# Kernel optimization log

Measured on AMD Instinct MI355X. Metric: run time of the kernel, lower is better.

## Reference

```python
import jax, jax.numpy as jnp
import numpy as np

B, T, D, H, C = 64, 256, 512, 1024, 1000

def setup_inputs() -> dict:
    key = jax.random.key(0)
    ks = jax.random.split(key, 6)
    s = 1.0 / np.sqrt(H)  # torch nn.RNN init scale
    return {
        "x": jax.random.normal(ks[0], (B, T, D), dtype=jnp.float32),
        "w_ih0": jax.random.normal(ks[1], (H, D), dtype=jnp.float32) * s,
        "w_hh0": jax.random.normal(ks[2], (H, H), dtype=jnp.float32) * s,
        "w_ih1": jax.random.normal(ks[3], (H, H), dtype=jnp.float32) * s,
        "w_hh1": jax.random.normal(ks[4], (H, H), dtype=jnp.float32) * s,
        "w_fc": jax.random.normal(ks[5], (C, H), dtype=jnp.float32) * s,
    }

def _rnn_layer(inp, w_ih, w_hh):
    # inp: [B, T, Din]; ReLU RNN, no bias (matches nn.RNN(nonlinearity='relu', bias=False))
    xs = jnp.einsum('btd,hd->tbh', inp, w_ih)  # precompute input projections for all steps
    h0 = jnp.zeros((inp.shape[0], w_hh.shape[0]), dtype=inp.dtype)
    def step(h, x_t):
        h = jax.nn.relu(x_t + h @ w_hh.T)
        return h, h
    _, ys = jax.lax.scan(step, h0, xs)  # ys: [T, B, H]
    return jnp.swapaxes(ys, 0, 1)  # [B, T, H]

def reference(x, w_ih0, w_hh0, w_ih1, w_hh1, w_fc):
    h1 = _rnn_layer(x, w_ih0, w_hh0)
    h2 = _rnn_layer(h1, w_ih1, w_hh1)
    # fc on last timestep, no bias
    return h2[:, -1, :] @ w_fc.T  # [B, C]
```

## Files before the change

### kernel.cpp

```cpp
#include <hip/hip_runtime.h>

#define T_STEPS 256
#define BATCH   64
#define HID     1024
#define DIN     512
#define NCLS    1000
#define NBLK    128
#define HSZ     (BATCH * HID)

typedef __attribute__((ext_vector_type(8))) short  short8;
typedef __attribute__((ext_vector_type(4))) float  f32x4;

__device__ __forceinline__ unsigned short rne_bf16(float f) {
    unsigned int u = __builtin_bit_cast(unsigned int, f);
    u += 0x7FFFu + ((u >> 16) & 1u);
    return (unsigned short)(u >> 16);
}
__device__ __forceinline__ float bf16_to_f(unsigned short h) {
    unsigned int u = ((unsigned int)h) << 16;
    return __builtin_bit_cast(float, u);
}

#define MFMA(a, b, c) __builtin_amdgcn_mfma_f32_16x16x32_bf16((a), (b), (c), 0, 0, 0)

__device__ __forceinline__ void grid_bar(int* cnt, int* gen, int bid, int tid, int p) {
    __syncthreads();
    if (tid == 0) {
        __threadfence();
        __hip_atomic_fetch_add(&cnt[(bid & 7) * 32], 1,
                               __ATOMIC_RELAXED, __HIP_MEMORY_SCOPE_AGENT);
        if (bid == 0) {
            const int target = NBLK * (p + 1);
            for (long it = 0; it < 1000000L; ++it) {
                int s = 0;
#pragma unroll
                for (int i = 0; i < 8; ++i)
                    s += __hip_atomic_load(&cnt[i * 32], __ATOMIC_RELAXED,
                                           __HIP_MEMORY_SCOPE_AGENT);
                if (s >= target) break;
                __builtin_amdgcn_s_sleep(1);
            }
            __threadfence();
            __hip_atomic_store(gen, p + 1, __ATOMIC_RELAXED, __HIP_MEMORY_SCOPE_AGENT);
        } else {
            for (long it = 0; it < 1000000L; ++it) {
                if (__hip_atomic_load(gen, __ATOMIC_RELAXED,
                                      __HIP_MEMORY_SCOPE_AGENT) >= p + 1)
                    break;
                __builtin_amdgcn_s_sleep(1);
            }
            __threadfence();
        }
    }
    __syncthreads();
}

__device__ __forceinline__ void reduce_store(const float* red, int tid,
                                             int mbase, int nbase,
                                             unsigned short* ohi, unsigned short* olo,
                                             float* of, const float* xp) {
    const int m = tid >> 4;
    const int n = (tid * 2) & 31;
    float s0, s1;
    if (xp) {
        float2 xi = *(const float2*)(xp + (size_t)(mbase + m) * HID + nbase + n);
        s0 = xi.x; s1 = xi.y;
    } else { s0 = 0.f; s1 = 0.f; }
#pragma unroll
    for (int ww = 0; ww < 8; ++ww) {
        const float* rp = red + ww * 1088 + m * 34 + n;
        s0 += rp[0];
        s1 += rp[1];
    }
    const float v0 = fmaxf(s0, 0.f), v1 = fmaxf(s1, 0.f);
    const unsigned short h0 = rne_bf16(v0), h1 = rne_bf16(v1);
    const unsigned int hp = (unsigned int)h0 | ((unsigned int)h1 << 16);
    const unsigned int lp = (unsigned int)rne_bf16(v0 - bf16_to_f(h0)) |
                            ((unsigned int)rne_bf16(v1 - bf16_to_f(h1)) << 16);
    const size_t o = (size_t)(mbase + m) * HID + nbase + n;
    *(unsigned int*)(ohi + o) = hp;
    *(unsigned int*)(olo + o) = lp;
    if (of) { float2 f2; f2.x = v0; f2.y = v1; *(float2*)(of + o) = f2; }
}

__global__ __launch_bounds__(512, 2)
void rnn_mfma(const float* __restrict__ xproj,
              const unsigned short* __restrict__ whh0h, const unsigned short* __restrict__ whh0l,
              const unsigned short* __restrict__ wih1h, const unsigned short* __restrict__ wih1l,
              const unsigned short* __restrict__ whh1h, const unsigned short* __restrict__ whh1l,
              unsigned short* h1hi, unsigned short* h1lo,
              unsigned short* h2hi, unsigned short* h2lo,
              float* h2f, int* bar) {
    __shared__ float red[8 * 1088];

    const int bid   = blockIdx.x;
    const int z     = bid >> 6;
    const int r     = bid & 63;
    const int nbase = (r >> 1) * 32;
    const int mbase = (r & 1) * 32;
    const int tid   = threadIdx.x;
    const int w     = tid >> 6;
    const int lane  = tid & 63;
    const int l15   = lane & 15;
    const int kq    = (lane >> 4) * 8;

    int* cnt = bar;
    int* gen = bar + 256;

    if (z == 0) {
        short8 WH[2][4], WL[2][4];
        const int kb = w * 128;
#pragma unroll
        for (int c = 0; c < 4; ++c)
#pragma unroll
            for (int nt = 0; nt < 2; ++nt) {
                const size_t o = (size_t)(nbase + nt * 16 + l15) * HID + kb + c * 32 + kq;
                WH[nt][c] = *(const short8*)(whh0h + o);
                WL[nt][c] = *(const short8*)(whh0l + o);
            }
        for (int p = 0; p <= T_STEPS; ++p) {
            if (p < T_STEPS) {
                f32x4 acc[2][2] = {};
                const unsigned short* hch = h1hi + (size_t)(p & 1) * HSZ;
                const unsigned short* hcl = h1lo + (size_t)(p & 1) * HSZ;
#pragma unroll
                for (int c = 0; c < 4; ++c) {
                    short8 ah[2], al[2];
#pragma unroll
                    for (int mt = 0; mt < 2; ++mt) {
                        const size_t o = (size_t)(mbase + mt * 16 + l15) * HID + kb + c * 32 + kq;
                        ah[mt] = *(const short8*)(hch + o);
                        al[mt] = *(const short8*)(hcl + o);
                    }
#pragma unroll
                    for (int mt = 0; mt < 2; ++mt)
#pragma unroll
                        for (int nt = 0; nt < 2; ++nt) {
                            acc[mt][nt] = MFMA(ah[mt], WH[nt][c], acc[mt][nt]);
                            acc[mt][nt] = MFMA(al[mt], WH[nt][c], acc[mt][nt]);
                            acc[mt][nt] = MFMA(ah[mt], WL[nt][c], acc[mt][nt]);
                        }
                }
#pragma unroll
                for (int mt = 0; mt < 2; ++mt)
#pragma unroll
                    for (int nt = 0; nt < 2; ++nt)
#pragma unroll
                        for (int i = 0; i < 4; ++i)
                            red[w * 1088 + (mt * 16 + (lane >> 4) * 4 + i) * 34 +
                                nt * 16 + l15] = acc[mt][nt][i];
                __syncthreads();
                const size_t ob = (size_t)((p + 1) & 1) * HSZ;
                reduce_store(red, tid, mbase, nbase, h1hi + ob, h1lo + ob, nullptr,
                             xproj + (size_t)p * BATCH * HID);
            }
            grid_bar(cnt, gen, bid, tid, p);
        }
    } else {
        short8 WH[2][8], WL[2][8];
        const unsigned short* ph = (w < 4) ? wih1h : whh1h;
        const unsigned short* pl = (w < 4) ? wih1l : whh1l;
        const int kb = (w & 3) * 256;
#pragma unroll
        for (int c = 0; c < 8; ++c)
#pragma unroll
            for (int nt = 0; nt < 2; ++nt) {
                const size_t o = (size_t)(nbase + nt * 16 + l15) * HID + kb + c * 32 + kq;
                WH[nt][c] = *(const short8*)(ph + o);
                WL[nt][c] = *(const short8*)(pl + o);
            }
        for (int p = 0; p <= T_STEPS; ++p) {
            if (p >= 1) {
                f32x4 acc[2][2] = {};
                const unsigned short* ash = (w < 4) ? h1hi + (size_t)(p & 1) * HSZ
                                                    : h2hi + (size_t)((p - 1) & 1) * HSZ;
                const unsigned short* asl = (w < 4) ? h1lo + (size_t)(p & 1) * HSZ
                                                    : h2lo + (size_t)((p - 1) & 1) * HSZ;
#pragma unroll
                for (int c = 0; c < 8; ++c) {
                    short8 ah[2], al[2];
#pragma unroll
                    for (int mt = 0; mt < 2; ++mt) {
                        const size_t o = (size_t)(mbase + mt * 16 + l15) * HID + kb + c * 32 + kq;
                        ah[mt] = *(const short8*)(ash + o);
                        al[mt] = *(const short8*)(asl + o);
                    }
#pragma unroll
                    for (int mt = 0; mt < 2; ++mt)
#pragma unroll
                        for (int nt = 0; nt < 2; ++nt) {
                            acc[mt][nt] = MFMA(ah[mt], WH[nt][c], acc[mt][nt]);
                            acc[mt][nt] = MFMA(al[mt], WH[nt][c], acc[mt][nt]);
                            acc[mt][nt] = MFMA(ah[mt], WL[nt][c], acc[mt][nt]);
                        }
                }
#pragma unroll
                for (int mt = 0; mt < 2; ++mt)
#pragma unroll
                    for (int nt = 0; nt < 2; ++nt)
#pragma unroll
                        for (int i = 0; i < 4; ++i)
                            red[w * 1088 + (mt * 16 + (lane >> 4) * 4 + i) * 34 +
                                nt * 16 + l15] = acc[mt][nt][i];
                __syncthreads();
                const size_t ob = (size_t)(p & 1) * HSZ;
                reduce_store(red, tid, mbase, nbase, h2hi + ob, h2lo + ob,
                             (p == T_STEPS) ? h2f : nullptr, nullptr);
            }
            grid_bar(cnt, gen, bid, tid, p);
        }
    }
}

__global__ __launch_bounds__(512)
void xproj_gemm(const float* __restrict__ x,
                const unsigned short* __restrict__ wh,
                const unsigned short* __restrict__ wl,
                float* __restrict__ xproj) {
    const int t    = blockIdx.x;
    const int nq   = blockIdx.y;
    const int w    = threadIdx.x >> 6;
    const int lane = threadIdx.x & 63;
    const int l15  = lane & 15;
    const int kq   = (lane >> 4) * 8;
    const int n0   = nq * 256 + w * 32;

    f32x4 acc[4][2] = {};
    for (int c = 0; c < 16; ++c) {
        const int k = c * 32 + kq;
        short8 wfh[2], wfl[2];
#pragma unroll
        for (int nt = 0; nt < 2; ++nt) {
            const size_t o = (size_t)(n0 + nt * 16 + l15) * DIN + k;
            wfh[nt] = *(const short8*)(wh + o);
            wfl[nt] = *(const short8*)(wl + o);
        }
#pragma unroll
        for (int mt = 0; mt < 4; ++mt) {
            const float* xr = x + ((size_t)(mt * 16 + l15) * T_STEPS + t) * DIN + k;
            float4 a0 = *(const float4*)xr;
            float4 a1 = *(const float4*)(xr + 4);
            float f[8] = {a0.x, a0.y, a0.z, a0.w, a1.x, a1.y, a1.z, a1.w};
            short8 ah, al;
#pragma unroll
            for (int i = 0; i < 8; ++i) {
                unsigned short h = rne_bf16(f[i]);
                ah[i] = (short)h;
                al[i] = (short)rne_bf16(f[i] - bf16_to_f(h));
            }
#pragma unroll
            for (int nt = 0; nt < 2; ++nt) {
                acc[mt][nt] = MFMA(ah, wfh[nt], acc[mt][nt]);
                acc[mt][nt] = MFMA(al, wfh[nt], acc[mt][nt]);
                acc[mt][nt] = MFMA(ah, wfl[nt], acc[mt][nt]);
            }
        }
    }
    float* op = xproj + (size_t)t * BATCH * HID;
#pragma unroll
    for (int mt = 0; mt < 4; ++mt)
#pragma unroll
        for (int nt = 0; nt < 2; ++nt)
#pragma unroll
            for (int i = 0; i < 4; ++i) {
                const int m = mt * 16 + (lane >> 4) * 4 + i;
                const int n = n0 + nt * 16 + l15;
                op[(size_t)m * HID + n] = acc[mt][nt][i];
            }
}

__global__ void split_w(const float* __restrict__ src,
                        unsigned short* __restrict__ hi,
                        unsigned short* __restrict__ lo, int n) {
    int i = blockIdx.x * 256 + threadIdx.x;
    if (i < n) {
        float v = src[i];
        unsigned short h = rne_bf16(v);
        hi[i] = h;
        lo[i] = rne_bf16(v - bf16_to_f(h));
    }
}

__global__ void zero_kernel(int* __restrict__ p, int n) {
    int i = blockIdx.x * 256 + threadIdx.x;
    if (i < n) p[i] = 0;
}

__global__ void fc_kernel(const float* __restrict__ h2,
                          const float* __restrict__ w_fc,
                          float* __restrict__ out) {
    __shared__ float hs[HID];
    const int b = blockIdx.x;
    for (int i = threadIdx.x; i < HID; i += 256) hs[i] = h2[(size_t)b * HID + i];
    __syncthreads();
    const int c = blockIdx.y * 256 + threadIdx.x;
    if (c < NCLS) {
        const float* w = w_fc + (size_t)c * HID;
        float s = 0.f;
        for (int k = 0; k < HID; k += 4) {
            float4 wv = *(const float4*)(w + k);
            s += wv.x * hs[k] + wv.y * hs[k + 1] + wv.z * hs[k + 2] + wv.w * hs[k + 3];
        }
        out[(size_t)b * NCLS + c] = s;
    }
}

extern "C" void kernel_launch(void* const* d_in, const int* in_sizes, int n_in,
                              void* d_out, int out_size, void* d_ws, size_t ws_size,
                              hipStream_t stream) {
    const float* x     = (const float*)d_in[0];
    const float* w_ih0 = (const float*)d_in[1];
    const float* w_hh0 = (const float*)d_in[2];
    const float* w_ih1 = (const float*)d_in[3];
    const float* w_hh1 = (const float*)d_in[4];
    const float* w_fc  = (const float*)d_in[5];
    float* out = (float*)d_out;

    char* ws = (char*)d_ws;
    size_t off = 0;
    auto alloc = [&](size_t bytes) { char* p = ws + off; off += bytes; return p; };
    float*          xproj = (float*)alloc((size_t)T_STEPS * BATCH * HID * 4);
    unsigned short* wih0h = (unsigned short*)alloc((size_t)DIN * HID * 2);
    unsigned short* wih0l = (unsigned short*)alloc((size_t)DIN * HID * 2);
    unsigned short* whh0h = (unsigned short*)alloc((size_t)HID * HID * 2);
    unsigned short* whh0l = (unsigned short*)alloc((size_t)HID * HID * 2);
    unsigned short* wih1h = (unsigned short*)alloc((size_t)HID * HID * 2);
    unsigned short* wih1l = (unsigned short*)alloc((size_t)HID * HID * 2);
    unsigned short* whh1h = (unsigned short*)alloc((size_t)HID * HID * 2);
    unsigned short* whh1l = (unsigned short*)alloc((size_t)HID * HID * 2);
    unsigned short* h1hi  = (unsigned short*)alloc(2 * HSZ * 2);
    unsigned short* h1lo  = (unsigned short*)alloc(2 * HSZ * 2);
    unsigned short* h2hi  = (unsigned short*)alloc(2 * HSZ * 2);
    unsigned short* h2lo  = (unsigned short*)alloc(2 * HSZ * 2);
    float*          h2f   = (float*)alloc(HSZ * 4);
    int*            bar   = (int*)alloc(4096);

    split_w<<<(DIN * HID + 255) / 256, 256, 0, stream>>>(w_ih0, wih0h, wih0l, DIN * HID);
    split_w<<<(HID * HID + 255) / 256, 256, 0, stream>>>(w_hh0, whh0h, whh0l, HID * HID);
    split_w<<<(HID * HID + 255) / 256, 256, 0, stream>>>(w_ih1, wih1h, wih1l, HID * HID);
    split_w<<<(HID * HID + 255) / 256, 256, 0, stream>>>(w_hh1, whh1h, whh1l, HID * HID);

    xproj_gemm<<<dim3(T_STEPS, 4), 512, 0, stream>>>(x, wih0h, wih0l, xproj);

    const int nzero = (4 * (2 * HSZ * 2) + HSZ * 4 + 4096) / 4;
    zero_kernel<<<(nzero + 255) / 256, 256, 0, stream>>>((int*)h1hi, nzero);

    rnn_mfma<<<NBLK, 512, 0, stream>>>(xproj,
                                       whh0h, whh0l,
                                       wih1h, wih1l, whh1h, whh1l,
                                       h1hi, h1lo, h2hi, h2lo, h2f, bar);

    fc_kernel<<<dim3(64, 4), 256, 0, stream>>>(h2f, w_fc, out);
}
```

Measured before the change: 3.981 ms.

## Replace grid-barrier fences with coherent atomic loads/stores and pin weight registers

```diff
diff --git a/kernel.cpp b/kernel.cpp
--- a/kernel.cpp
+++ b/kernel.cpp
@@ -10,6 +10,7 @@
 
 typedef __attribute__((ext_vector_type(8))) short  short8;
 typedef __attribute__((ext_vector_type(4))) float  f32x4;
+typedef __attribute__((ext_vector_type(4))) int    i32x4;
 
 __device__ __forceinline__ unsigned short rne_bf16(float f) {
     unsigned int u = __builtin_bit_cast(unsigned int, f);
@@ -22,16 +23,29 @@
 }
 
 #define MFMA(a, b, c) __builtin_amdgcn_mfma_f32_16x16x32_bf16((a), (b), (c), 0, 0, 0)
+#define PIN(v) asm volatile("" : "+v"(v))
+
+__device__ __forceinline__ short8 ld_coh8(const unsigned short* p) {
+    unsigned int* q = (unsigned int*)p;
+    union { unsigned int u[4]; short8 s; } r;
+    r.u[0] = __hip_atomic_load(q + 0, __ATOMIC_RELAXED, __HIP_MEMORY_SCOPE_AGENT);
+    r.u[1] = __hip_atomic_load(q + 1, __ATOMIC_RELAXED, __HIP_MEMORY_SCOPE_AGENT);
+    r.u[2] = __hip_atomic_load(q + 2, __ATOMIC_RELAXED, __HIP_MEMORY_SCOPE_AGENT);
+    r.u[3] = __hip_atomic_load(q + 3, __ATOMIC_RELAXED, __HIP_MEMORY_SCOPE_AGENT);
+    return r.s;
+}
+__device__ __forceinline__ void st_coh(unsigned short* p, unsigned int v) {
+    __hip_atomic_store((unsigned int*)p, v, __ATOMIC_RELAXED, __HIP_MEMORY_SCOPE_AGENT);
+}
 
 __device__ __forceinline__ void grid_bar(int* cnt, int* gen, int bid, int tid, int p) {
     __syncthreads();
     if (tid == 0) {
-        __threadfence();
         __hip_atomic_fetch_add(&cnt[(bid & 7) * 32], 1,
                                __ATOMIC_RELAXED, __HIP_MEMORY_SCOPE_AGENT);
         if (bid == 0) {
             const int target = NBLK * (p + 1);
-            for (long it = 0; it < 1000000L; ++it) {
+            for (long it = 0; it < 2000000L; ++it) {
                 int s = 0;
 #pragma unroll
                 for (int i = 0; i < 8; ++i)
@@ -40,16 +54,14 @@
                 if (s >= target) break;
                 __builtin_amdgcn_s_sleep(1);
             }
-            __threadfence();
             __hip_atomic_store(gen, p + 1, __ATOMIC_RELAXED, __HIP_MEMORY_SCOPE_AGENT);
         } else {
-            for (long it = 0; it < 1000000L; ++it) {
+            for (long it = 0; it < 2000000L; ++it) {
                 if (__hip_atomic_load(gen, __ATOMIC_RELAXED,
                                       __HIP_MEMORY_SCOPE_AGENT) >= p + 1)
                     break;
                 __builtin_amdgcn_s_sleep(1);
             }
-            __threadfence();
         }
     }
     __syncthreads();
@@ -78,8 +90,8 @@
     const unsigned int lp = (unsigned int)rne_bf16(v0 - bf16_to_f(h0)) |
                             ((unsigned int)rne_bf16(v1 - bf16_to_f(h1)) << 16);
     const size_t o = (size_t)(mbase + m) * HID + nbase + n;
-    *(unsigned int*)(ohi + o) = hp;
-    *(unsigned int*)(olo + o) = lp;
+    st_coh(ohi + o, hp);
+    st_coh(olo + o, lp);
     if (of) { float2 f2; f2.x = v0; f2.y = v1; *(float2*)(of + o) = f2; }
 }
 
@@ -108,15 +120,17 @@
     int* gen = bar + 256;
 
     if (z == 0) {
-        short8 WH[2][4], WL[2][4];
+        i32x4 WH[2][4], WL[2][4];
         const int kb = w * 128;
 #pragma unroll
         for (int c = 0; c < 4; ++c)
 #pragma unroll
             for (int nt = 0; nt < 2; ++nt) {
                 const size_t o = (size_t)(nbase + nt * 16 + l15) * HID + kb + c * 32 + kq;
-                WH[nt][c] = *(const short8*)(whh0h + o);
-                WL[nt][c] = *(const short8*)(whh0l + o);
+                WH[nt][c] = *(const i32x4*)(whh0h + o);
+                WL[nt][c] = *(const i32x4*)(whh0l + o);
+                PIN(WH[nt][c]);
+                PIN(WL[nt][c]);
             }
         for (int p = 0; p <= T_STEPS; ++p) {
             if (p < T_STEPS) {
@@ -129,16 +143,16 @@
 #pragma unroll
                     for (int mt = 0; mt < 2; ++mt) {
                         const size_t o = (size_t)(mbase + mt * 16 + l15) * HID + kb + c * 32 + kq;
-                        ah[mt] = *(const short8*)(hch + o);
-                        al[mt] = *(const short8*)(hcl + o);
+                        ah[mt] = ld_coh8(hch + o);
+                        al[mt] = ld_coh8(hcl + o);
                     }
 #pragma unroll
                     for (int mt = 0; mt < 2; ++mt)
 #pragma unroll
                         for (int nt = 0; nt < 2; ++nt) {
-                            acc[mt][nt] = MFMA(ah[mt], WH[nt][c], acc[mt][nt]);
-                            acc[mt][nt] = MFMA(al[mt], WH[nt][c], acc[mt][nt]);
-                            acc[mt][nt] = MFMA(ah[mt], WL[nt][c], acc[mt][nt]);
+                            acc[mt][nt] = MFMA(ah[mt], __builtin_bit_cast(short8, WH[nt][c]), acc[mt][nt]);
+                            acc[mt][nt] = MFMA(al[mt], __builtin_bit_cast(short8, WH[nt][c]), acc[mt][nt]);
+                            acc[mt][nt] = MFMA(ah[mt], __builtin_bit_cast(short8, WL[nt][c]), acc[mt][nt]);
                         }
                 }
 #pragma unroll
@@ -157,7 +171,7 @@
             grid_bar(cnt, gen, bid, tid, p);
         }
     } else {
-        short8 WH[2][8], WL[2][8];
+        i32x4 WH[2][8], WL[2][8];
         const unsigned short* ph = (w < 4) ? wih1h : whh1h;
         const unsigned short* pl = (w < 4) ? wih1l : whh1l;
         const int kb = (w & 3) * 256;
@@ -166,8 +180,10 @@
 #pragma unroll
             for (int nt = 0; nt < 2; ++nt) {
                 const size_t o = (size_t)(nbase + nt * 16 + l15) * HID + kb + c * 32 + kq;
-                WH[nt][c] = *(const short8*)(ph + o);
-                WL[nt][c] = *(const short8*)(pl + o);
+                WH[nt][c] = *(const i32x4*)(ph + o);
+                WL[nt][c] = *(const i32x4*)(pl + o);
+                PIN(WH[nt][c]);
+                PIN(WL[nt][c]);
             }
         for (int p = 0; p <= T_STEPS; ++p) {
             if (p >= 1) {
@@ -182,16 +198,16 @@
 #pragma unroll
                     for (int mt = 0; mt < 2; ++mt) {
                         const size_t o = (size_t)(mbase + mt * 16 + l15) * HID + kb + c * 32 + kq;
-                        ah[mt] = *(const short8*)(ash + o);
-                        al[mt] = *(const short8*)(asl + o);
+                        ah[mt] = ld_coh8(ash + o);
+                        al[mt] = ld_coh8(asl + o);
                     }
 #pragma unroll
                     for (int mt = 0; mt < 2; ++mt)
 #pragma unroll
                         for (int nt = 0; nt < 2; ++nt) {
-                            acc[mt][nt] = MFMA(ah[mt], WH[nt][c], acc[mt][nt]);
-                            acc[mt][nt] = MFMA(al[mt], WH[nt][c], acc[mt][nt]);
-                            acc[mt][nt] = MFMA(ah[mt], WL[nt][c], acc[mt][nt]);
+                            acc[mt][nt] = MFMA(ah[mt], __builtin_bit_cast(short8, WH[nt][c]), acc[mt][nt]);
+                            acc[mt][nt] = MFMA(al[mt], __builtin_bit_cast(short8, WH[nt][c]), acc[mt][nt]);
+                            acc[mt][nt] = MFMA(ah[mt], __builtin_bit_cast(short8, WL[nt][c]), acc[mt][nt]);
                         }
                 }
 #pragma unroll
```

Result: slower. 7.854 ms (+97.3%).

## Split persistent RNN into three roles across 192 blocks with LDS-resident weights

Applied to the files above, without the earlier changes.

```diff
diff --git a/kernel.cpp b/kernel.cpp
--- a/kernel.cpp
+++ b/kernel.cpp
@@ -5,7 +5,8 @@
 #define HID     1024
 #define DIN     512
 #define NCLS    1000
-#define NBLK    128
+#define NBLK    192
+#define PH_LAST 257
 #define HSZ     (BATCH * HID)
 
 typedef __attribute__((ext_vector_type(8))) short  short8;
@@ -31,7 +32,7 @@
                                __ATOMIC_RELAXED, __HIP_MEMORY_SCOPE_AGENT);
         if (bid == 0) {
             const int target = NBLK * (p + 1);
-            for (long it = 0; it < 1000000L; ++it) {
+            for (long it = 0; it < 2000000L; ++it) {
                 int s = 0;
 #pragma unroll
                 for (int i = 0; i < 8; ++i)
@@ -43,7 +44,7 @@
             __threadfence();
             __hip_atomic_store(gen, p + 1, __ATOMIC_RELAXED, __HIP_MEMORY_SCOPE_AGENT);
         } else {
-            for (long it = 0; it < 1000000L; ++it) {
+            for (long it = 0; it < 2000000L; ++it) {
                 if (__hip_atomic_load(gen, __ATOMIC_RELAXED,
                                       __HIP_MEMORY_SCOPE_AGENT) >= p + 1)
                     break;
@@ -53,34 +54,6 @@
         }
     }
     __syncthreads();
-}
-
-__device__ __forceinline__ void reduce_store(const float* red, int tid,
-                                             int mbase, int nbase,
-                                             unsigned short* ohi, unsigned short* olo,
-                                             float* of, const float* xp) {
-    const int m = tid >> 4;
-    const int n = (tid * 2) & 31;
-    float s0, s1;
-    if (xp) {
-        float2 xi = *(const float2*)(xp + (size_t)(mbase + m) * HID + nbase + n);
-        s0 = xi.x; s1 = xi.y;
-    } else { s0 = 0.f; s1 = 0.f; }
-#pragma unroll
-    for (int ww = 0; ww < 8; ++ww) {
-        const float* rp = red + ww * 1088 + m * 34 + n;
-        s0 += rp[0];
-        s1 += rp[1];
-    }
-    const float v0 = fmaxf(s0, 0.f), v1 = fmaxf(s1, 0.f);
-    const unsigned short h0 = rne_bf16(v0), h1 = rne_bf16(v1);
-    const unsigned int hp = (unsigned int)h0 | ((unsigned int)h1 << 16);
-    const unsigned int lp = (unsigned int)rne_bf16(v0 - bf16_to_f(h0)) |
-                            ((unsigned int)rne_bf16(v1 - bf16_to_f(h1)) << 16);
-    const size_t o = (size_t)(mbase + m) * HID + nbase + n;
-    *(unsigned int*)(ohi + o) = hp;
-    *(unsigned int*)(olo + o) = lp;
-    if (of) { float2 f2; f2.x = v0; f2.y = v1; *(float2*)(of + o) = f2; }
 }
 
 __global__ __launch_bounds__(512, 2)
@@ -90,125 +63,108 @@
               const unsigned short* __restrict__ whh1h, const unsigned short* __restrict__ whh1l,
               unsigned short* h1hi, unsigned short* h1lo,
               unsigned short* h2hi, unsigned short* h2lo,
-              float* h2f, int* bar) {
-    __shared__ float red[8 * 1088];
-
-    const int bid   = blockIdx.x;
-    const int z     = bid >> 6;
-    const int r     = bid & 63;
-    const int nbase = (r >> 1) * 32;
-    const int mbase = (r & 1) * 32;
-    const int tid   = threadIdx.x;
-    const int w     = tid >> 6;
-    const int lane  = tid & 63;
-    const int l15   = lane & 15;
-    const int kq    = (lane >> 4) * 8;
-
+              float* ubuf, float* redg, float* h2f, int* bar) {
+    __shared__ short wlds[32 * 2 * 64 * 8];
+
+    const int bid  = blockIdx.x;
+    const int role = bid >> 6;
+    const int n0   = (bid & 63) * 16;
+    const int tid  = threadIdx.x;
+    const int w    = tid >> 6;
+    const int lane = tid & 63;
+    const int l15  = lane & 15;
+    const int q    = lane >> 4;
+    const int s    = w >> 1;
+    const int msub = w & 1;
+
+    const unsigned short* Wh = role == 0 ? whh0h : role == 1 ? wih1h : whh1h;
+    const unsigned short* Wl = role == 0 ? whh0l : role == 1 ? wih1l : whh1l;
+
+    for (int idx = tid; idx < 4096; idx += 512) {
+        const int ln = idx & 63, hl = (idx >> 6) & 1, kc = idx >> 7;
+        const unsigned short* src = (hl ? Wl : Wh) +
+            (size_t)(n0 + (ln & 15)) * 1024 + kc * 32 + (ln >> 4) * 8;
+        *(short8*)&wlds[((kc * 2 + hl) * 64 + ln) * 8] = *(const short8*)src;
+    }
+    __syncthreads();
+
+    float* redB = redg + (size_t)bid * 4096;
     int* cnt = bar;
     int* gen = bar + 256;
 
-    if (z == 0) {
-        short8 WH[2][4], WL[2][4];
-        const int kb = w * 128;
-#pragma unroll
-        for (int c = 0; c < 4; ++c)
-#pragma unroll
-            for (int nt = 0; nt < 2; ++nt) {
-                const size_t o = (size_t)(nbase + nt * 16 + l15) * HID + kb + c * 32 + kq;
-                WH[nt][c] = *(const short8*)(whh0h + o);
-                WL[nt][c] = *(const short8*)(whh0l + o);
-            }
-        for (int p = 0; p <= T_STEPS; ++p) {
-            if (p < T_STEPS) {
-                f32x4 acc[2][2] = {};
-                const unsigned short* hch = h1hi + (size_t)(p & 1) * HSZ;
-                const unsigned short* hcl = h1lo + (size_t)(p & 1) * HSZ;
-#pragma unroll
-                for (int c = 0; c < 4; ++c) {
-                    short8 ah[2], al[2];
-#pragma unroll
-                    for (int mt = 0; mt < 2; ++mt) {
-                        const size_t o = (size_t)(mbase + mt * 16 + l15) * HID + kb + c * 32 + kq;
-                        ah[mt] = *(const short8*)(hch + o);
-                        al[mt] = *(const short8*)(hcl + o);
-                    }
-#pragma unroll
-                    for (int mt = 0; mt < 2; ++mt)
-#pragma unroll
-                        for (int nt = 0; nt < 2; ++nt) {
-                            acc[mt][nt] = MFMA(ah[mt], WH[nt][c], acc[mt][nt]);
-                            acc[mt][nt] = MFMA(al[mt], WH[nt][c], acc[mt][nt]);
-                            acc[mt][nt] = MFMA(ah[mt], WL[nt][c], acc[mt][nt]);
-                        }
-                }
-#pragma unroll
-                for (int mt = 0; mt < 2; ++mt)
-#pragma unroll
-                    for (int nt = 0; nt < 2; ++nt)
-#pragma unroll
-                        for (int i = 0; i < 4; ++i)
-                            red[w * 1088 + (mt * 16 + (lane >> 4) * 4 + i) * 34 +
-                                nt * 16 + l15] = acc[mt][nt][i];
-                __syncthreads();
+    for (int p = 0; p <= PH_LAST; ++p) {
+        const bool active = (role == 0) ? (p < T_STEPS)
+                          : (role == 1) ? (p >= 1 && p <= T_STEPS)
+                                        : (p >= 2);
+        if (active) {
+            const unsigned short* Ah = (role == 2 ? h2hi : h1hi) + (size_t)(p & 1) * HSZ;
+            const unsigned short* Al = (role == 2 ? h2lo : h1lo) + (size_t)(p & 1) * HSZ;
+            f32x4 acc[2] = {};
+#pragma unroll
+            for (int c = 0; c < 8; ++c) {
+                const int kc = s * 8 + c;
+                const int ko = kc * 32 + q * 8;
+                const short8 wh = *(const short8*)&wlds[((kc * 2 + 0) * 64 + lane) * 8];
+                const short8 wl = *(const short8*)&wlds[((kc * 2 + 1) * 64 + lane) * 8];
+                const size_t r0 = (size_t)(msub * 32 + l15) * 1024 + ko;
+                const size_t r1 = (size_t)(msub * 32 + 16 + l15) * 1024 + ko;
+                short8 ah0 = *(const short8*)(Ah + r0);
+                short8 al0 = *(const short8*)(Al + r0);
+                short8 ah1 = *(const short8*)(Ah + r1);
+                short8 al1 = *(const short8*)(Al + r1);
+                acc[0] = MFMA(ah0, wh, acc[0]);
+                acc[0] = MFMA(al0, wh, acc[0]);
+                acc[0] = MFMA(ah0, wl, acc[0]);
+                acc[1] = MFMA(ah1, wh, acc[1]);
+                acc[1] = MFMA(al1, wh, acc[1]);
+                acc[1] = MFMA(ah1, wl, acc[1]);
+            }
+#pragma unroll
+            for (int mt = 0; mt < 2; ++mt)
+#pragma unroll
+                for (int i = 0; i < 4; ++i)
+                    redB[s * 1024 + (msub * 32 + mt * 16 + q * 4 + i) * 16 + l15] =
+                        acc[mt][i];
+        }
+        __syncthreads();
+        if (active) {
+            const int m  = tid >> 3;
+            const int nl = (tid & 7) * 2;
+            float s0 = 0.f, s1 = 0.f;
+#pragma unroll
+            for (int ss = 0; ss < 4; ++ss) {
+                float2 r = *(const float2*)&redB[ss * 1024 + m * 16 + nl];
+                s0 += r.x; s1 += r.y;
+            }
+            const size_t o = (size_t)m * HID + n0 + nl;
+            if (role == 0) {
+                float2 xp = *(const float2*)(xproj + (size_t)p * HSZ + o);
+                const float v0 = fmaxf(s0 + xp.x, 0.f);
+                const float v1 = fmaxf(s1 + xp.y, 0.f);
+                const unsigned short g0 = rne_bf16(v0), g1 = rne_bf16(v1);
                 const size_t ob = (size_t)((p + 1) & 1) * HSZ;
-                reduce_store(red, tid, mbase, nbase, h1hi + ob, h1lo + ob, nullptr,
-                             xproj + (size_t)p * BATCH * HID);
-            }
-            grid_bar(cnt, gen, bid, tid, p);
-        }
-    } else {
-        short8 WH[2][8], WL[2][8];
-        const unsigned short* ph = (w < 4) ? wih1h : whh1h;
-        const unsigned short* pl = (w < 4) ? wih1l : whh1l;
-        const int kb = (w & 3) * 256;
-#pragma unroll
-        for (int c = 0; c < 8; ++c)
-#pragma unroll
-            for (int nt = 0; nt < 2; ++nt) {
-                const size_t o = (size_t)(nbase + nt * 16 + l15) * HID + kb + c * 32 + kq;
-                WH[nt][c] = *(const short8*)(ph + o);
-                WL[nt][c] = *(const short8*)(pl + o);
-            }
-        for (int p = 0; p <= T_STEPS; ++p) {
-            if (p >= 1) {
-                f32x4 acc[2][2] = {};
-                const unsigned short* ash = (w < 4) ? h1hi + (size_t)(p & 1) * HSZ
-                                                    : h2hi + (size_t)((p - 1) & 1) * HSZ;
-                const unsigned short* asl = (w < 4) ? h1lo + (size_t)(p & 1) * HSZ
-                                                    : h2lo + (size_t)((p - 1) & 1) * HSZ;
-#pragma unroll
-                for (int c = 0; c < 8; ++c) {
-                    short8 ah[2], al[2];
-#pragma unroll
-                    for (int mt = 0; mt < 2; ++mt) {
-                        const size_t o = (size_t)(mbase + mt * 16 + l15) * HID + kb + c * 32 + kq;
-                        ah[mt] = *(const short8*)(ash + o);
-                        al[mt] = *(const short8*)(asl + o);
-                    }
-#pragma unroll
-                    for (int mt = 0; mt < 2; ++mt)
-#pragma unroll
-                        for (int nt = 0; nt < 2; ++nt) {
-                            acc[mt][nt] = MFMA(ah[mt], WH[nt][c], acc[mt][nt]);
-                            acc[mt][nt] = MFMA(al[mt], WH[nt][c], acc[mt][nt]);
-                            acc[mt][nt] = MFMA(ah[mt], WL[nt][c], acc[mt][nt]);
-                        }
-                }
-#pragma unroll
-                for (int mt = 0; mt < 2; ++mt)
-#pragma unroll
-                    for (int nt = 0; nt < 2; ++nt)
-#pragma unroll
-                        for (int i = 0; i < 4; ++i)
-                            red[w * 1088 + (mt * 16 + (lane >> 4) * 4 + i) * 34 +
-                                nt * 16 + l15] = acc[mt][nt][i];
-                __syncthreads();
-                const size_t ob = (size_t)(p & 1) * HSZ;
-                reduce_store(red, tid, mbase, nbase, h2hi + ob, h2lo + ob,
-                             (p == T_STEPS) ? h2f : nullptr, nullptr);
-            }
-            grid_bar(cnt, gen, bid, tid, p);
-        }
+                *(unsigned int*)(h1hi + ob + o) = (unsigned int)g0 | ((unsigned int)g1 << 16);
+                *(unsigned int*)(h1lo + ob + o) =
+                    (unsigned int)rne_bf16(v0 - bf16_to_f(g0)) |
+                    ((unsigned int)rne_bf16(v1 - bf16_to_f(g1)) << 16);
+            } else if (role == 1) {
+                float2 uv; uv.x = s0; uv.y = s1;
+                *(float2*)(ubuf + (size_t)(p & 1) * HSZ + o) = uv;
+            } else {
+                float2 uv = *(const float2*)(ubuf + (size_t)((p - 1) & 1) * HSZ + o);
+                const float v0 = fmaxf(s0 + uv.x, 0.f);
+                const float v1 = fmaxf(s1 + uv.y, 0.f);
+                const unsigned short g0 = rne_bf16(v0), g1 = rne_bf16(v1);
+                const size_t ob = (size_t)((p - 1) & 1) * HSZ;
+                *(unsigned int*)(h2hi + ob + o) = (unsigned int)g0 | ((unsigned int)g1 << 16);
+                *(unsigned int*)(h2lo + ob + o) =
+                    (unsigned int)rne_bf16(v0 - bf16_to_f(g0)) |
+                    ((unsigned int)rne_bf16(v1 - bf16_to_f(g1)) << 16);
+                if (p == PH_LAST) { float2 f2; f2.x = v0; f2.y = v1;
+                                    *(float2*)(h2f + o) = f2; }
+            }
+        }
+        grid_bar(cnt, gen, bid, tid, p);
     }
 }
 
@@ -328,10 +284,12 @@
     unsigned short* wih1l = (unsigned short*)alloc((size_t)HID * HID * 2);
     unsigned short* whh1h = (unsigned short*)alloc((size_t)HID * HID * 2);
     unsigned short* whh1l = (unsigned short*)alloc((size_t)HID * HID * 2);
+    float*          redg  = (float*)alloc((size_t)NBLK * 4096 * 4);
     unsigned short* h1hi  = (unsigned short*)alloc(2 * HSZ * 2);
     unsigned short* h1lo  = (unsigned short*)alloc(2 * HSZ * 2);
     unsigned short* h2hi  = (unsigned short*)alloc(2 * HSZ * 2);
     unsigned short* h2lo  = (unsigned short*)alloc(2 * HSZ * 2);
+    float*          ubuf  = (float*)alloc(2 * HSZ * 4);
     float*          h2f   = (float*)alloc(HSZ * 4);
     int*            bar   = (int*)alloc(4096);
 
@@ -342,13 +300,13 @@
 
     xproj_gemm<<<dim3(T_STEPS, 4), 512, 0, stream>>>(x, wih0h, wih0l, xproj);
 
-    const int nzero = (4 * (2 * HSZ * 2) + HSZ * 4 + 4096) / 4;
+    const int nzero = (4 * (2 * HSZ * 2) + 2 * HSZ * 4 + HSZ * 4 + 4096) / 4;
     zero_kernel<<<(nzero + 255) / 256, 256, 0, stream>>>((int*)h1hi, nzero);
 
     rnn_mfma<<<NBLK, 512, 0, stream>>>(xproj,
-                                       whh0h, whh0l,
-                                       wih1h, wih1l, whh1h, whh1l,
-                                       h1hi, h1lo, h2hi, h2lo, h2f, bar);
+                                       whh0h, whh0l, wih1h, wih1l, whh1h, whh1l,
+                                       h1hi, h1lo, h2hi, h2lo,
+                                       ubuf, redg, h2f, bar);
 
     fc_kernel<<<dim3(64, 4), 256, 0, stream>>>(h2f, w_fc, out);
 }
```

New measurement: 5.775 ms. 45.1% more time.
